# Performance work log

Hardware: AMD Instinct MI355X
Metric: run time of the kernel (lower is better)

## Reference

```python
import jax, jax.numpy as jnp
import numpy as np

M = 12      # max_context_size
H = 768     # hidden_size
NH = 8      # global encoder heads
HD = H // NH
FF = 2048   # global encoder ff_dim
B = 8192


def _gather_hist(buf, mask, idx, ctx):
    """Age-sorted gather of valid circular-buffer slots (oldest first), padded to ctx."""
    Bb, Mx, Hh = buf.shape
    pos = jnp.arange(Mx)
    age = (idx[:, None] - pos[None, :]) % Mx              # [B,M] age of each slot
    key = jnp.where(mask, -age, Mx + 1)                   # valid slots first, oldest (max age) first
    order = jnp.argsort(key, axis=1)                      # stable sort, matches python sorted()
    sorted_buf = jnp.take_along_axis(buf, order[:, :, None], axis=1)
    nvalid = mask.sum(axis=1)                             # [B]
    hist = sorted_buf[:, :ctx]                            # [B,ctx,H]
    valid = jnp.arange(ctx)[None, :] < nvalid[:, None]
    hist = hist * valid[:, :, None]                       # zero out padding rows
    return hist, jnp.minimum(nvalid, ctx)


def _seq_with_current(buf, mask, idx, z_k, ctx):
    """History (ctx-1 slots) + current utterance at the last position (faithful to original,
    including the original's padding-mask behavior arange >= hist_len+1)."""
    Bb = z_k.shape[0]
    hist, hlen = _gather_hist(buf, mask, idx, ctx - 1)
    seq = jnp.concatenate([hist, jnp.zeros((Bb, 1, buf.shape[-1]), buf.dtype)], axis=1)
    seq = seq.at[:, ctx - 1].set(z_k)
    lengths = jnp.minimum(hlen + 1, ctx)
    pad = jnp.arange(ctx)[None, :] >= lengths[:, None]    # True = padded
    return seq, lengths, pad


def _layernorm(x, g, b):
    mu = x.mean(-1, keepdims=True)
    var = x.var(-1, keepdims=True)
    return (x - mu) * jax.lax.rsqrt(var + 1e-5) * g + b


def _forward(z_k, context_buffer, buffer_mask, buffer_indices,
             Wq, bq, Wk, bk, Wv, bv, Wo, bo, ln1_g, ln1_b,
             W1, b1, W2, b2, ln2_g, ln2_b, Wd, bd, Wl, bl, Wg, bg):
    mask = buffer_mask.astype(bool)
    idx = buffer_indices.astype(jnp.int32)
    Bb = z_k.shape[0]

    # ---- global path: 12-slot context -> post-LN transformer layer -> masked mean pool
    gseq, glen, gpad = _seq_with_current(context_buffer, mask, idx, z_k, 12)
    S = 12
    q = (gseq @ Wq + bq).reshape(Bb, S, NH, HD)
    k = (gseq @ Wk + bk).reshape(Bb, S, NH, HD)
    v = (gseq @ Wv + bv).reshape(Bb, S, NH, HD)
    scores = jnp.einsum('bqhd,bkhd->bhqk', q, k) / np.sqrt(HD).astype(np.float32)
    scores = jnp.where(gpad[:, None, None, :], jnp.float32(-1e9), scores)
    attn = jax.nn.softmax(scores, axis=-1)
    ao = jnp.einsum('bhqk,bkhd->bqhd', attn, v).reshape(Bb, S, H) @ Wo + bo
    x = _layernorm(gseq + ao, ln1_g, ln1_b)
    ff = jax.nn.relu(x @ W1 + b1) @ W2 + b2
    x = _layernorm(x + ff, ln2_g, ln2_b)
    gvalid = (~gpad).astype(x.dtype)                       # [B,12]
    denom = jnp.maximum(gvalid.sum(1, keepdims=True), 1.0)
    x_g = (x * gvalid[:, :, None]).sum(1) / denom          # [B,H]

    # ---- direct path
    x_d = jnp.tanh(z_k @ Wd + bd)

    # ---- local path: 5-slot context -> masked mean pool -> projection
    lseq, llen, lpad = _seq_with_current(context_buffer, mask, idx, z_k, 5)
    lvalid = (~lpad).astype(lseq.dtype)
    ldenom = jnp.maximum(lvalid.sum(1, keepdims=True), 1.0)
    lpool = (lseq * lvalid[:, :, None]).sum(1) / ldenom
    x_l = jnp.tanh(lpool @ Wl + bl)

    # ---- gate over [direct, local, global]
    paths = jnp.stack([x_d, x_l, x_g], axis=1)             # [B,3,H]
    logits = paths.reshape(Bb, 3 * H) @ Wg + bg            # [B,3]
    gate = jax.nn.softmax(logits, axis=-1)
    h_k = jnp.einsum('br,brh->bh', gate, paths)
    return h_k


def setup_inputs() -> dict:
    key = jax.random.key(0)
    ks = jax.random.split(key, 24)
    s = 0.02
    inp = {
        'z_k': jax.random.normal(ks[0], (B, H), jnp.float32),
        'context_buffer': jax.random.normal(ks[1], (B, M, H), jnp.float32),
        'buffer_mask': jax.random.randint(ks[2], (B, M), 0, 2, jnp.int32),
        'buffer_indices': jax.random.randint(ks[3], (B,), 0, M, jnp.int32),
        'Wq': jax.random.normal(ks[4], (H, H), jnp.float32) * s,
        'bq': jnp.zeros((H,), jnp.float32),
        'Wk': jax.random.normal(ks[5], (H, H), jnp.float32) * s,
        'bk': jnp.zeros((H,), jnp.float32),
        'Wv': jax.random.normal(ks[6], (H, H), jnp.float32) * s,
        'bv': jnp.zeros((H,), jnp.float32),
        'Wo': jax.random.normal(ks[7], (H, H), jnp.float32) * s,
        'bo': jnp.zeros((H,), jnp.float32),
        'ln1_g': jnp.ones((H,), jnp.float32),
        'ln1_b': jnp.zeros((H,), jnp.float32),
        'W1': jax.random.normal(ks[8], (H, FF), jnp.float32) * s,
        'b1': jnp.zeros((FF,), jnp.float32),
        'W2': jax.random.normal(ks[9], (FF, H), jnp.float32) * s,
        'b2': jnp.zeros((H,), jnp.float32),
        'ln2_g': jnp.ones((H,), jnp.float32),
        'ln2_b': jnp.zeros((H,), jnp.float32),
        'Wd': jax.random.normal(ks[10], (H, H), jnp.float32) * s,
        'bd': jnp.zeros((H,), jnp.float32),
        'Wl': jax.random.normal(ks[11], (H, H), jnp.float32) * s,
        'bl': jnp.zeros((H,), jnp.float32),
        'Wg': jax.random.normal(ks[12], (3 * H, 3), jnp.float32) * s,
        'bg': jnp.zeros((3,), jnp.float32),
    }
    return inp


def reference(z_k, context_buffer, buffer_mask, buffer_indices,
              Wq, bq, Wk, bk, Wv, bv, Wo, bo, ln1_g, ln1_b,
              W1, b1, W2, b2, ln2_g, ln2_b, Wd, bd, Wl, bl, Wg, bg):
    return _forward(z_k, context_buffer, buffer_mask, buffer_indices,
                    Wq, bq, Wk, bk, Wv, bv, Wo, bo, ln1_g, ln1_b,
                    W1, b1, W2, b2, ln2_g, ln2_b, Wd, bd, Wl, bl, Wg, bg)
```

## Files before the change

### kernel.cpp

```cpp
#include <hip/hip_runtime.h>
#include <cstdint>
#include <cstddef>

typedef __bf16 bf16;
typedef __attribute__((ext_vector_type(8))) __bf16 bf16x8;
typedef __attribute__((ext_vector_type(4))) float f32x4;

#define B_TOT 8192

__device__ __forceinline__ void gload16(const void* g, void* l) {
  __builtin_amdgcn_global_load_lds(
      (__attribute__((address_space(1))) void*)g,
      (__attribute__((address_space(3))) void*)l, 16, 0, 0);
}

__device__ __forceinline__ void block_sum2(float& a, float& b, float* lds8) {
#pragma unroll
  for (int o = 32; o; o >>= 1) {
    a += __shfl_xor(a, o, 64);
    b += __shfl_xor(b, o, 64);
  }
  int w = threadIdx.x >> 6;
  if ((threadIdx.x & 63) == 0) { lds8[w] = a; lds8[4 + w] = b; }
  __syncthreads();
  a = lds8[0] + lds8[1] + lds8[2] + lds8[3];
  b = lds8[4] + lds8[5] + lds8[6] + lds8[7];
  __syncthreads();
}

__global__ __launch_bounds__(256) void scan1_kernel(
    const int* __restrict__ mask, int* __restrict__ Lg, int* __restrict__ lbase,
    int* __restrict__ btot, int b0)
{
  __shared__ int ts[256];
  const int t = threadIdx.x;
  const int b = blockIdx.x * 256 + t;
  const int* mp = mask + (long)(b0 + b) * 12;
  int nv = 0;
#pragma unroll
  for (int p = 0; p < 12; ++p) nv += (mp[p] != 0);
  int L = (nv < 11 ? nv : 11) + 1;
  ts[t] = L;
  __syncthreads();
  for (int o = 1; o < 256; o <<= 1) {
    int v = (t >= o) ? ts[t - o] : 0;
    __syncthreads();
    ts[t] += v;
    __syncthreads();
  }
  Lg[b] = L;
  lbase[b] = ts[t] - L;
  if (t == 255) btot[blockIdx.x] = ts[255];
}

__global__ __launch_bounds__(64) void scan2_kernel(
    const int* __restrict__ btot, int* __restrict__ boff, int* __restrict__ meta, int nb)
{
  if (threadIdx.x == 0) {
    int acc = 0;
    for (int i = 0; i < nb; ++i) { int v = btot[i]; boff[i] = acc; acc += v; }
    meta[0] = acc;
  }
}

__global__ __launch_bounds__(256) void prep_kernel(
    const float* __restrict__ z, const float* __restrict__ buf,
    const int* __restrict__ mask, const int* __restrict__ idxs,
    const int* __restrict__ lbase, const int* __restrict__ boff,
    int* __restrict__ fbase, bf16* __restrict__ gseq,
    bf16* __restrict__ zl, int b0, int Bc)
{
  const int bl = blockIdx.x;
  const int b  = b0 + bl;
  __shared__ int ord[12];
  __shared__ int s_nv;
  if (threadIdx.x == 0) {
    int id = idxs[b];
    int nv = 0;
    for (int a = 11; a >= 0; --a) {
      int pos = id - a; if (pos < 0) pos += 12;
      if (mask[b * 12 + pos]) ord[nv++] = pos;
    }
    s_nv = nv;
  }
  const long bs = (long)lbase[bl] + boff[bl >> 8];
  if (threadIdx.x == 0) fbase[bl] = (int)bs;
  __syncthreads();
  const int nv = s_nv;
  const int hg = (nv < 11 ? nv : 11);
  const int hl = (nv < 4 ? nv : 4);
  const float ld = 1.0f / (float)(hl + 1);
  for (int c = threadIdx.x; c < 768; c += 256) {
    float zv = z[(long)b * 768 + c];
    zl[(long)bl * 768 + c] = (bf16)zv;
    float ls = 0.0f;
    for (int s = 0; s < hg; ++s) {
      float v = buf[((long)b * 12 + ord[s]) * 768 + c];
      gseq[(bs + s) * 768 + c] = (bf16)v;
      if (s < hl) ls += v;
    }
    gseq[(bs + hg) * 768 + c] = (hg == 11) ? (bf16)zv : (bf16)0.0f;
    if (nv >= 4) ls += zv;
    zl[((long)Bc + bl) * 768 + c] = (bf16)(ls * ld);
  }
}

__global__ __launch_bounds__(256) void transpose_bf16(
    const float* __restrict__ W, bf16* __restrict__ Wt, int K, int N)
{
  __shared__ float tile[32][33];
  int bn = blockIdx.x * 32;
  int bk = blockIdx.y * 32;
  int tx = threadIdx.x & 31;
  int ty0 = threadIdx.x >> 5;
  for (int ty = ty0; ty < 32; ty += 8)
    tile[ty][tx] = W[(long)(bk + ty) * N + bn + tx];
  __syncthreads();
  for (int ty = ty0; ty < 32; ty += 8)
    Wt[(long)(bn + ty) * K + bk + tx] = (bf16)tile[tx][ty];
}

__global__ __launch_bounds__(256) void pack3_kernel(
    const float* __restrict__ a, const float* __restrict__ b,
    const float* __restrict__ c, float* __restrict__ out)
{
  int t = blockIdx.x * blockDim.x + threadIdx.x;
  if (t < 768) out[t] = a[t];
  else if (t < 1536) out[t] = b[t - 768];
  else if (t < 2304) out[t] = c[t - 1536];
}

__global__ __launch_bounds__(256, 2) void gemm_bt(
    const bf16* __restrict__ A, const bf16* __restrict__ Bt,
    const float* __restrict__ bias, void* __restrict__ C,
    int K, int N, int act, int outf32,
    const int* __restrict__ mlim, int msplit,
    const bf16* __restrict__ Bt2, const float* __restrict__ bias2)
{
  __shared__ __align__(16) bf16 smem[2 * 128 * 64];
  bf16* As = smem;
  bf16* Bs = smem + 128 * 64;
  int gx = gridDim.x, gy = gridDim.y;
  int bx = blockIdx.x, by = blockIdx.y;
  if ((gy & 7) == 0) {
    int l = bx + gx * by;
    int xcd = l & 7, slot = l >> 3;
    bx = slot % gx;
    by = (slot / gx) * 8 + xcd;
  }
  const long m0 = (long)by * 128;
  const long n0 = (long)bx * 128;
  if (mlim && m0 >= mlim[0]) return;
  const bf16* Bsel = (m0 >= msplit) ? Bt2 : Bt;
  const float* bsel = (m0 >= msplit) ? bias2 : bias;

  const int tid  = threadIdx.x;
  const int wave = tid >> 6;
  const int lane = tid & 63;
  const int wm = (wave >> 1) * 64;
  const int wn = (wave & 1) * 64;
  const int i16  = lane & 15;
  const int quad = lane >> 4;
  const int l8 = lane >> 3;
  const int c7 = lane & 7;

  const int csrc = c7 ^ l8;
  const bf16* Ag[4]; const bf16* Bg[4];
  bf16* Al[4]; bf16* Bl[4];
#pragma unroll
  for (int u = 0; u < 4; ++u) {
    int r = wave * 32 + u * 8 + l8;
    Ag[u] = A    + (m0 + r) * K + csrc * 8;
    Bg[u] = Bsel + (n0 + r) * K + csrc * 8;
    Al[u] = As + (wave * 32 + u * 8) * 64 + lane * 8;
    Bl[u] = Bs + (wave * 32 + u * 8) * 64 + lane * 8;
  }

  f32x4 acc[4][4] = {};

  for (int kt = 0; kt < K; kt += 64) {
    __syncthreads();
#pragma unroll
    for (int u = 0; u < 4; ++u) {
      gload16(Ag[u] + kt, Al[u]);
      gload16(Bg[u] + kt, Bl[u]);
    }
    __syncthreads();
#pragma unroll
    for (int s = 0; s < 2; ++s) {
      const int cofs = ((s << 2) | quad) ^ c7;
      bf16x8 af[4], bfr[4];
#pragma unroll
      for (int i = 0; i < 4; ++i)
        af[i] = *(const bf16x8*)(As + (wm + i * 16 + i16) * 64 + cofs * 8);
#pragma unroll
      for (int j = 0; j < 4; ++j)
        bfr[j] = *(const bf16x8*)(Bs + (wn + j * 16 + i16) * 64 + cofs * 8);
#pragma unroll
      for (int i = 0; i < 4; ++i)
#pragma unroll
        for (int j = 0; j < 4; ++j)
          acc[i][j] = __builtin_amdgcn_mfma_f32_16x16x32_bf16(af[i], bfr[j], acc[i][j], 0, 0, 0);
    }
  }

  if (!outf32) {
    __syncthreads();
    bf16* Cs = smem;
#pragma unroll
    for (int j = 0; j < 4; ++j) {
      int col = wn + j * 16 + i16;
      int c8s = (col >> 3) ^ (quad << 1);
      int clo = col & 7;
      float bv = bsel[n0 + col];
#pragma unroll
      for (int i = 0; i < 4; ++i) {
#pragma unroll
        for (int r = 0; r < 4; ++r) {
          int row = wm + i * 16 + quad * 4 + r;
          float v = acc[i][j][r] + bv;
          if (act == 1) v = fmaxf(v, 0.0f);
          Cs[row * 128 + c8s * 8 + clo] = (bf16)v;
        }
      }
    }
    __syncthreads();
    bf16* Cg = (bf16*)C;
#pragma unroll
    for (int u = 0; u < 8; ++u) {
      int g = u * 256 + tid;
      int row = g >> 4, c8 = g & 15;
      int c8s = c8 ^ (((row >> 2) & 3) << 1);
      *(bf16x8*)(Cg + (m0 + row) * N + n0 + c8 * 8) =
          *(const bf16x8*)(Cs + row * 128 + c8s * 8);
    }
  } else {
#pragma unroll
    for (int i = 0; i < 4; ++i) {
#pragma unroll
      for (int j = 0; j < 4; ++j) {
        long col = n0 + wn + j * 16 + i16;
        float bv = bsel[col];
#pragma unroll
        for (int r = 0; r < 4; ++r) {
          long row = m0 + wm + i * 16 + quad * 4 + r;
          float v = acc[i][j][r] + bv;
          if (act == 1) v = fmaxf(v, 0.0f);
          else if (act == 2) v = tanhf(v);
          ((float*)C)[row * N + col] = v;
        }
      }
    }
  }
}

__global__ __launch_bounds__(256, 8) void attn_kernel(
    const bf16* __restrict__ QKV, const int* __restrict__ fbase,
    const int* __restrict__ Lg, bf16* __restrict__ AO)
{
  const int bl  = blockIdx.x;
  const int tid = threadIdx.x;
  const int L   = Lg[bl];
  const long bs = fbase[bl];
  const bf16* qb = QKV + bs * 2304;
  __shared__ bf16 kx[12 * 768];
  __shared__ float att[8][12][12];
  const int LC = L * 96;
  for (int t = tid; t < LC; t += 256) {
    int s = t / 96, c8 = t - s * 96;
    *(bf16x8*)(kx + s * 768 + ((c8 ^ (s & 7)) << 3)) =
        *(const bf16x8*)(qb + (long)s * 2304 + 768 + (c8 << 3));
  }
  __syncthreads();
  const int LL = L * L;
  for (int t = tid; t < 8 * LL; t += 256) {
    int h = t / LL, r = t - h * LL, i = r / L, j = r - (r / L) * L;
    const bf16x8* q = (const bf16x8*)(qb + (long)i * 2304 + h * 96);
    const bf16* kr = kx + j * 768;
    const int cb = h * 12;
    const int jx = j & 7;
    float a = 0.0f;
#pragma unroll
    for (int d = 0; d < 12; ++d) {
      bf16x8 qa = q[d];
      bf16x8 ka = *(const bf16x8*)(kr + (((cb + d) ^ jx) << 3));
#pragma unroll
      for (int e = 0; e < 8; ++e) a += (float)qa[e] * (float)ka[e];
    }
    att[h][i][j] = a * 0.10206207261596575f;
  }
  __syncthreads();
  for (int t = tid; t < 8 * L; t += 256) {
    int h = t / L, i = t - (t / L) * L;
    float mx = -3e38f;
    for (int j = 0; j < L; ++j) mx = fmaxf(mx, att[h][i][j]);
    float sum = 0.0f;
    for (int j = 0; j < L; ++j) { float e = __expf(att[h][i][j] - mx); att[h][i][j] = e; sum += e; }
    float inv = 1.0f / sum;
    for (int j = 0; j < L; ++j) att[h][i][j] *= inv;
  }
  __syncthreads();
  for (int t = tid; t < LC; t += 256) {
    int i = t / 96, c8 = t - i * 96;
    int h = c8 / 12;
    const bf16* vp = qb + 1536 + (c8 << 3);
    float acc[8] = {};
    for (int j = 0; j < L; ++j) {
      float a = att[h][i][j];
      bf16x8 vv = *(const bf16x8*)(vp + (long)j * 2304);
#pragma unroll
      for (int e = 0; e < 8; ++e) acc[e] += a * (float)vv[e];
    }
    bf16x8 o;
#pragma unroll
    for (int e = 0; e < 8; ++e) o[e] = (bf16)acc[e];
    *(bf16x8*)(AO + (bs + i) * 768 + (c8 << 3)) = o;
  }
}

__global__ __launch_bounds__(256) void ln1_kernel(
    const bf16* __restrict__ WoO, const bf16* __restrict__ gseq,
    const float* __restrict__ gam, const float* __restrict__ bet,
    bf16* __restrict__ X, const int* __restrict__ meta)
{
  const long row = blockIdx.x;
  if (row >= meta[0]) return;
  const int tid = threadIdx.x;
  __shared__ float red[8];
  float v[3]; float s = 0.0f, ss = 0.0f;
#pragma unroll
  for (int u = 0; u < 3; ++u) {
    int c = tid + u * 256;
    float x = (float)WoO[row * 768 + c] + (float)gseq[row * 768 + c];
    v[u] = x; s += x; ss += x * x;
  }
  block_sum2(s, ss, red);
  float mu  = s * (1.0f / 768.0f);
  float var = ss * (1.0f / 768.0f) - mu * mu;
  float inv = 1.0f / sqrtf(var + 1e-5f);
#pragma unroll
  for (int u = 0; u < 3; ++u) {
    int c = tid + u * 256;
    X[row * 768 + c] = (bf16)((v[u] - mu) * inv * gam[c] + bet[c]);
  }
}

__global__ __launch_bounds__(256) void ln2gate_kernel(
    const bf16* __restrict__ X, const bf16* __restrict__ FFo,
    const float* __restrict__ gam, const float* __restrict__ bet,
    const int* __restrict__ fbase, const int* __restrict__ Lg,
    const float* __restrict__ xdl, const float* __restrict__ Wg,
    const float* __restrict__ bg, float* __restrict__ out, int b0, int Bc)
{
  const int bl = blockIdx.x;
  const int tid = threadIdx.x;
  const int L = Lg[bl];
  const long bs = fbase[bl];
  __shared__ float red[8];
  __shared__ float red3[12];
  float p0 = 0.0f, p1 = 0.0f, p2 = 0.0f;
  for (int s = 0; s < L; ++s) {
    long row = bs + s;
    float v[3]; float sm = 0.0f, sq = 0.0f;
#pragma unroll
    for (int u = 0; u < 3; ++u) {
      int c = tid + u * 256;
      float x = (float)X[row * 768 + c] + (float)FFo[row * 768 + c];
      v[u] = x; sm += x; sq += x * x;
    }
    block_sum2(sm, sq, red);
    float mu  = sm * (1.0f / 768.0f);
    float var = sq * (1.0f / 768.0f) - mu * mu;
    float inv = 1.0f / sqrtf(var + 1e-5f);
    p0 += (v[0] - mu) * inv * gam[tid]       + bet[tid];
    p1 += (v[1] - mu) * inv * gam[tid + 256] + bet[tid + 256];
    p2 += (v[2] - mu) * inv * gam[tid + 512] + bet[tid + 512];
  }
  float dn = 1.0f / (float)L;
  p0 *= dn; p1 *= dn; p2 *= dn;
  const float* xd = xdl + (long)bl * 768;
  const float* xl = xdl + ((long)Bc + bl) * 768;
  float xd0 = xd[tid], xd1 = xd[tid + 256], xd2 = xd[tid + 512];
  float xl0 = xl[tid], xl1 = xl[tid + 256], xl2 = xl[tid + 512];
  float l0 = 0.0f, l1 = 0.0f, l2 = 0.0f;
#pragma unroll
  for (int r = 0; r < 3; ++r) {
    float lr = xd0 * Wg[tid * 3 + r] + xd1 * Wg[(tid + 256) * 3 + r] + xd2 * Wg[(tid + 512) * 3 + r]
             + xl0 * Wg[(768 + tid) * 3 + r] + xl1 * Wg[(1024 + tid) * 3 + r] + xl2 * Wg[(1280 + tid) * 3 + r]
             + p0 * Wg[(1536 + tid) * 3 + r] + p1 * Wg[(1792 + tid) * 3 + r] + p2 * Wg[(2048 + tid) * 3 + r];
    if (r == 0) l0 = lr; else if (r == 1) l1 = lr; else l2 = lr;
  }
#pragma unroll
  for (int o = 32; o; o >>= 1) {
    l0 += __shfl_xor(l0, o, 64);
    l1 += __shfl_xor(l1, o, 64);
    l2 += __shfl_xor(l2, o, 64);
  }
  if ((tid & 63) == 0) { int w = tid >> 6; red3[w * 3] = l0; red3[w * 3 + 1] = l1; red3[w * 3 + 2] = l2; }
  __syncthreads();
  l0 = red3[0] + red3[3] + red3[6] + red3[9]  + bg[0];
  l1 = red3[1] + red3[4] + red3[7] + red3[10] + bg[1];
  l2 = red3[2] + red3[5] + red3[8] + red3[11] + bg[2];
  float mx = fmaxf(l0, fmaxf(l1, l2));
  float e0 = __expf(l0 - mx), e1 = __expf(l1 - mx), e2 = __expf(l2 - mx);
  float inv = 1.0f / (e0 + e1 + e2);
  e0 *= inv; e1 *= inv; e2 *= inv;
  float* op = out + (long)(b0 + bl) * 768;
  op[tid]       = e0 * xd0 + e1 * xl0 + e2 * p0;
  op[tid + 256] = e0 * xd1 + e1 * xl1 + e2 * p1;
  op[tid + 512] = e0 * xd2 + e1 * xl2 + e2 * p2;
}

extern "C" void kernel_launch(void* const* d_in, const int* in_sizes, int n_in,
                              void* d_out, int out_size, void* d_ws, size_t ws_size,
                              hipStream_t stream) {
  const float* z    = (const float*)d_in[0];
  const float* buf  = (const float*)d_in[1];
  const int*   mask = (const int*)d_in[2];
  const int*   idxs = (const int*)d_in[3];
  const float* Wq = (const float*)d_in[4];  const float* bq = (const float*)d_in[5];
  const float* Wk = (const float*)d_in[6];  const float* bk = (const float*)d_in[7];
  const float* Wv = (const float*)d_in[8];  const float* bv = (const float*)d_in[9];
  const float* Wo = (const float*)d_in[10]; const float* bo = (const float*)d_in[11];
  const float* ln1g = (const float*)d_in[12]; const float* ln1b = (const float*)d_in[13];
  const float* W1 = (const float*)d_in[14]; const float* b1 = (const float*)d_in[15];
  const float* W2 = (const float*)d_in[16]; const float* b2 = (const float*)d_in[17];
  const float* ln2g = (const float*)d_in[18]; const float* ln2b = (const float*)d_in[19];
  const float* Wd = (const float*)d_in[20]; const float* bd = (const float*)d_in[21];
  const float* Wl = (const float*)d_in[22]; const float* blw = (const float*)d_in[23];
  const float* Wg = (const float*)d_in[24]; const float* bg = (const float*)d_in[25];
  float* out = (float*)d_out;
  (void)in_sizes; (void)n_in; (void)out_size;

  auto rnd = [](size_t x) { return (x + 255) & ~(size_t)255; };

  size_t fixed = 0;
  fixed += rnd((size_t)2304 * 768 * 2);
  fixed += rnd((size_t)768 * 768 * 2);
  fixed += rnd((size_t)2048 * 768 * 2);
  fixed += rnd((size_t)768 * 2048 * 2);
  fixed += rnd((size_t)768 * 768 * 2) * 2;
  fixed += rnd((size_t)2304 * 4) + 256 + 512 + 512;

  auto chunkBytes = [&](size_t bc) {
    return rnd((size_t)55296 * bc) + 3 * rnd((size_t)18432 * bc)
         + rnd((size_t)3072 * bc) + rnd((size_t)6144 * bc)
         + 3 * rnd((size_t)4 * bc);
  };
  int Bc = 8192;
  while (Bc > 1024 && fixed + chunkBytes(Bc) > ws_size) Bc >>= 1;

  size_t off = 0;
  auto alloc = [&](size_t n) { void* p = (char*)d_ws + off; off += rnd(n); return p; };
  bf16* Wqkv_t = (bf16*)alloc((size_t)2304 * 768 * 2);
  bf16* Wo_t   = (bf16*)alloc((size_t)768 * 768 * 2);
  bf16* W1_t   = (bf16*)alloc((size_t)2048 * 768 * 2);
  bf16* W2_t   = (bf16*)alloc((size_t)768 * 2048 * 2);
  bf16* Wd_t   = (bf16*)alloc((size_t)768 * 768 * 2);
  bf16* Wl_t   = (bf16*)alloc((size_t)768 * 768 * 2);
  float* bqkv  = (float*)alloc((size_t)2304 * 4);
  int*  meta   = (int*)alloc(256);
  int*  btot   = (int*)alloc(512);
  int*  boff   = (int*)alloc(512);
  bf16* P1 = (bf16*)alloc((size_t)55296 * Bc);
  bf16* P2 = (bf16*)alloc((size_t)18432 * Bc);
  bf16* P3 = (bf16*)alloc((size_t)18432 * Bc);
  bf16* P4 = (bf16*)alloc((size_t)18432 * Bc);
  bf16* zl   = (bf16*)alloc((size_t)3072 * Bc);
  float* xdl = (float*)alloc((size_t)6144 * Bc);
  int*  Lg    = (int*)alloc((size_t)4 * Bc);
  int*  lbase = (int*)alloc((size_t)4 * Bc);
  int*  fbase = (int*)alloc((size_t)4 * Bc);

  transpose_bf16<<<dim3(24, 24), 256, 0, stream>>>(Wq, Wqkv_t,                 768, 768);
  transpose_bf16<<<dim3(24, 24), 256, 0, stream>>>(Wk, Wqkv_t + 768 * 768,     768, 768);
  transpose_bf16<<<dim3(24, 24), 256, 0, stream>>>(Wv, Wqkv_t + 2 * 768 * 768, 768, 768);
  transpose_bf16<<<dim3(24, 24), 256, 0, stream>>>(Wo, Wo_t, 768, 768);
  transpose_bf16<<<dim3(64, 24), 256, 0, stream>>>(W1, W1_t, 768, 2048);
  transpose_bf16<<<dim3(24, 64), 256, 0, stream>>>(W2, W2_t, 2048, 768);
  transpose_bf16<<<dim3(24, 24), 256, 0, stream>>>(Wd, Wd_t, 768, 768);
  transpose_bf16<<<dim3(24, 24), 256, 0, stream>>>(Wl, Wl_t, 768, 768);
  pack3_kernel<<<9, 256, 0, stream>>>(bq, bk, bv, bqkv);

  const int BIG = 0x7fffffff;
  for (int b0 = 0; b0 < B_TOT; b0 += Bc) {
    const int Ycap = (12 * Bc) / 128;
    scan1_kernel<<<Bc / 256, 256, 0, stream>>>(mask, Lg, lbase, btot, b0);
    scan2_kernel<<<1, 64, 0, stream>>>(btot, boff, meta, Bc / 256);
    prep_kernel<<<Bc, 256, 0, stream>>>(z, buf, mask, idxs, lbase, boff, fbase, P2, zl, b0, Bc);
    gemm_bt<<<dim3(6, (2 * Bc) / 128), 256, 0, stream>>>(zl, Wd_t, bd, xdl, 768, 768, 2, 1, nullptr, Bc, Wl_t, blw);
    gemm_bt<<<dim3(18, Ycap), 256, 0, stream>>>(P2, Wqkv_t, bqkv, P1, 768, 2304, 0, 0, meta, BIG, nullptr, nullptr);
    attn_kernel<<<Bc, 256, 0, stream>>>(P1, fbase, Lg, P3);
    gemm_bt<<<dim3(6, Ycap), 256, 0, stream>>>(P3, Wo_t, bo, P4, 768, 768, 0, 0, meta, BIG, nullptr, nullptr);
    ln1_kernel<<<12 * Bc, 256, 0, stream>>>(P4, P2, ln1g, ln1b, P3, meta);
    gemm_bt<<<dim3(16, Ycap), 256, 0, stream>>>(P3, W1_t, b1, P1, 768, 2048, 1, 0, meta, BIG, nullptr, nullptr);
    gemm_bt<<<dim3(6, Ycap), 256, 0, stream>>>(P1, W2_t, b2, P2, 2048, 768, 0, 0, meta, BIG, nullptr, nullptr);
    ln2gate_kernel<<<Bc, 256, 0, stream>>>(P3, P2, ln2g, ln2b, fbase, Lg, xdl, Wg, bg, out, b0, Bc);
  }
}
```

Measured before the change: 1.499 ms.

## Replace 128x128 GEMM with 256x256-tile, 512-thread, multi-stage pipelined GEMM

Swaps the 256-thread 128x128-tile bf16 MFMA GEMM for a 512-thread kernel with 256x256 output tiles. The K loop now steps by 32 through a 4-deep LDS ring buffer, with up to three stages loaded ahead. Next-stage A and B loads are interleaved between the two MFMA halves, and the MFMA sections get raised wave priority. The aim is more operand reuse per byte loaded and better hiding of global-load latency. The cost is 128KB of LDS per block, so at most one block fits per CU. The larger tiles also mean fewer blocks and coarser padding waste on the variable-length M dimension.

```diff
diff --git a/kernel.cpp b/kernel.cpp
--- a/kernel.cpp
+++ b/kernel.cpp
@@ -130,16 +130,15 @@
   else if (t < 2304) out[t] = c[t - 1536];
 }
 
-__global__ __launch_bounds__(256, 2) void gemm_bt(
+__global__ __launch_bounds__(512, 2) void gemm256(
     const bf16* __restrict__ A, const bf16* __restrict__ Bt,
     const float* __restrict__ bias, void* __restrict__ C,
     int K, int N, int act, int outf32,
     const int* __restrict__ mlim, int msplit,
     const bf16* __restrict__ Bt2, const float* __restrict__ bias2)
 {
-  __shared__ __align__(16) bf16 smem[2 * 128 * 64];
-  bf16* As = smem;
-  bf16* Bs = smem + 128 * 64;
+  __shared__ __align__(16) bf16 smem[65536];
+  char* sb = (char*)smem;
   int gx = gridDim.x, gy = gridDim.y;
   int bx = blockIdx.x, by = blockIdx.y;
   if ((gy & 7) == 0) {
@@ -148,103 +147,132 @@
     bx = slot % gx;
     by = (slot / gx) * 8 + xcd;
   }
-  const long m0 = (long)by * 128;
-  const long n0 = (long)bx * 128;
+  const long m0 = (long)by * 256;
+  const long n0 = (long)bx * 256;
   if (mlim && m0 >= mlim[0]) return;
   const bf16* Bsel = (m0 >= msplit) ? Bt2 : Bt;
   const float* bsel = (m0 >= msplit) ? bias2 : bias;
 
   const int tid  = threadIdx.x;
+  const int lane = tid & 63;
   const int wave = tid >> 6;
-  const int lane = tid & 63;
-  const int wm = (wave >> 1) * 64;
-  const int wn = (wave & 1) * 64;
+  const int wm = (wave >> 2) * 128;
+  const int wn = (wave & 3) * 64;
   const int i16  = lane & 15;
   const int quad = lane >> 4;
-  const int l8 = lane >> 3;
-  const int c7 = lane & 7;
-
-  const int csrc = c7 ^ l8;
-  const bf16* Ag[4]; const bf16* Bg[4];
-  bf16* Al[4]; bf16* Bl[4];
-#pragma unroll
-  for (int u = 0; u < 4; ++u) {
-    int r = wave * 32 + u * 8 + l8;
-    Ag[u] = A    + (m0 + r) * K + csrc * 8;
-    Bg[u] = Bsel + (n0 + r) * K + csrc * 8;
-    Al[u] = As + (wave * 32 + u * 8) * 64 + lane * 8;
-    Bl[u] = Bs + (wave * 32 + u * 8) * 64 + lane * 8;
-  }
-
-  f32x4 acc[4][4] = {};
-
-  for (int kt = 0; kt < K; kt += 64) {
-    __syncthreads();
-#pragma unroll
-    for (int u = 0; u < 4; ++u) {
-      gload16(Ag[u] + kt, Al[u]);
-      gload16(Bg[u] + kt, Bl[u]);
-    }
-    __syncthreads();
-#pragma unroll
-    for (int s = 0; s < 2; ++s) {
-      const int cofs = ((s << 2) | quad) ^ c7;
-      bf16x8 af[4], bfr[4];
-#pragma unroll
-      for (int i = 0; i < 4; ++i)
-        af[i] = *(const bf16x8*)(As + (wm + i * 16 + i16) * 64 + cofs * 8);
-#pragma unroll
-      for (int j = 0; j < 4; ++j)
-        bfr[j] = *(const bf16x8*)(Bs + (wn + j * 16 + i16) * 64 + cofs * 8);
-#pragma unroll
-      for (int i = 0; i < 4; ++i)
-#pragma unroll
-        for (int j = 0; j < 4; ++j)
-          acc[i][j] = __builtin_amdgcn_mfma_f32_16x16x32_bf16(af[i], bfr[j], acc[i][j], 0, 0, 0);
-    }
+
+  const int sr = tid >> 2;
+  const int cA = (tid & 3) ^ ((sr >> 1) & 3);
+  const bf16* Ag0 = A    + (m0 + sr) * K + cA * 8;
+  const bf16* Ag1 = A    + (m0 + 128 + sr) * K + cA * 8;
+  const bf16* Bg0 = Bsel + (n0 + sr) * K + cA * 8;
+  const bf16* Bg1 = Bsel + (n0 + 128 + sr) * K + cA * 8;
+  const int ldst = tid << 4;
+
+  const int NK = K >> 5;
+  const int npre = NK < 3 ? NK : 3;
+  for (int s = 0; s < npre; ++s) {
+    char* as_ = sb + ((s & 3) << 14);
+    char* bs_ = sb + 65536 + ((s & 3) << 14);
+    gload16(Ag0 + s * 32, as_ + ldst);
+    gload16(Ag1 + s * 32, as_ + 8192 + ldst);
+    gload16(Bg0 + s * 32, bs_ + ldst);
+    gload16(Bg1 + s * 32, bs_ + 8192 + ldst);
+  }
+
+  const int fc = (quad ^ ((i16 >> 1) & 3)) << 4;
+  f32x4 acc[8][4] = {};
+
+  for (int s = 0; s < NK; ++s) {
+    const char* as_ = sb + ((s & 3) << 14);
+    const char* bs_ = sb + 65536 + ((s & 3) << 14);
+    asm volatile("s_waitcnt vmcnt(8)" ::: "memory");
+    __builtin_amdgcn_s_barrier();
+    bf16x8 a0[4], b0[4];
+#pragma unroll
+    for (int f = 0; f < 4; ++f)
+      a0[f] = *(const bf16x8*)(as_ + (wm + f * 16 + i16) * 64 + fc);
+#pragma unroll
+    for (int g = 0; g < 4; ++g)
+      b0[g] = *(const bf16x8*)(bs_ + (wn + g * 16 + i16) * 64 + fc);
+    if (s + 3 < NK) {
+      char* an = sb + (((s + 3) & 3) << 14);
+      gload16(Ag0 + (s + 3) * 32, an + ldst);
+      gload16(Ag1 + (s + 3) * 32, an + 8192 + ldst);
+    }
+    __builtin_amdgcn_s_barrier();
+    asm volatile("s_waitcnt lgkmcnt(0)" ::: "memory");
+    __builtin_amdgcn_sched_barrier(0);
+    __builtin_amdgcn_s_setprio(1);
+#pragma unroll
+    for (int f = 0; f < 4; ++f)
+#pragma unroll
+      for (int g = 0; g < 4; ++g)
+        acc[f][g] = __builtin_amdgcn_mfma_f32_16x16x32_bf16(a0[f], b0[g], acc[f][g], 0, 0, 0);
+    __builtin_amdgcn_s_setprio(0);
+    __builtin_amdgcn_s_barrier();
+    bf16x8 a1[4];
+#pragma unroll
+    for (int f = 0; f < 4; ++f)
+      a1[f] = *(const bf16x8*)(as_ + (wm + (f + 4) * 16 + i16) * 64 + fc);
+    if (s + 3 < NK) {
+      char* bn = sb + 65536 + (((s + 3) & 3) << 14);
+      gload16(Bg0 + (s + 3) * 32, bn + ldst);
+      gload16(Bg1 + (s + 3) * 32, bn + 8192 + ldst);
+    }
+    __builtin_amdgcn_s_barrier();
+    asm volatile("s_waitcnt lgkmcnt(0)" ::: "memory");
+    __builtin_amdgcn_sched_barrier(0);
+    __builtin_amdgcn_s_setprio(1);
+#pragma unroll
+    for (int f = 0; f < 4; ++f)
+#pragma unroll
+      for (int g = 0; g < 4; ++g)
+        acc[f + 4][g] = __builtin_amdgcn_mfma_f32_16x16x32_bf16(a1[f], b0[g], acc[f + 4][g], 0, 0, 0);
+    __builtin_amdgcn_s_setprio(0);
   }
 
   if (!outf32) {
     __syncthreads();
     bf16* Cs = smem;
 #pragma unroll
-    for (int j = 0; j < 4; ++j) {
-      int col = wn + j * 16 + i16;
+    for (int g = 0; g < 4; ++g) {
+      int col = wn + g * 16 + i16;
       int c8s = (col >> 3) ^ (quad << 1);
       int clo = col & 7;
       float bv = bsel[n0 + col];
 #pragma unroll
-      for (int i = 0; i < 4; ++i) {
+      for (int f = 0; f < 8; ++f) {
 #pragma unroll
         for (int r = 0; r < 4; ++r) {
-          int row = wm + i * 16 + quad * 4 + r;
-          float v = acc[i][j][r] + bv;
+          int row = wm + f * 16 + quad * 4 + r;
+          float v = acc[f][g][r] + bv;
           if (act == 1) v = fmaxf(v, 0.0f);
-          Cs[row * 128 + c8s * 8 + clo] = (bf16)v;
+          Cs[row * 256 + c8s * 8 + clo] = (bf16)v;
         }
       }
     }
     __syncthreads();
     bf16* Cg = (bf16*)C;
 #pragma unroll
-    for (int u = 0; u < 8; ++u) {
-      int g = u * 256 + tid;
-      int row = g >> 4, c8 = g & 15;
+    for (int u = 0; u < 16; ++u) {
+      int g = u * 512 + tid;
+      int row = g >> 5, c8 = g & 31;
       int c8s = c8 ^ (((row >> 2) & 3) << 1);
       *(bf16x8*)(Cg + (m0 + row) * N + n0 + c8 * 8) =
-          *(const bf16x8*)(Cs + row * 128 + c8s * 8);
+          *(const bf16x8*)(Cs + row * 256 + c8s * 8);
     }
   } else {
 #pragma unroll
-    for (int i = 0; i < 4; ++i) {
-#pragma unroll
-      for (int j = 0; j < 4; ++j) {
-        long col = n0 + wn + j * 16 + i16;
+    for (int f = 0; f < 8; ++f) {
+#pragma unroll
+      for (int g = 0; g < 4; ++g) {
+        long col = n0 + wn + g * 16 + i16;
         float bv = bsel[col];
 #pragma unroll
         for (int r = 0; r < 4; ++r) {
-          long row = m0 + wm + i * 16 + quad * 4 + r;
-          float v = acc[i][j][r] + bv;
+          long row = m0 + wm + f * 16 + quad * 4 + r;
+          float v = acc[f][g][r] + bv;
           if (act == 1) v = fmaxf(v, 0.0f);
           else if (act == 2) v = tanhf(v);
           ((float*)C)[row * N + col] = v;
@@ -484,17 +512,17 @@
 
   const int BIG = 0x7fffffff;
   for (int b0 = 0; b0 < B_TOT; b0 += Bc) {
-    const int Ycap = (12 * Bc) / 128;
+    const int Ycap = (12 * Bc) / 256;
     scan1_kernel<<<Bc / 256, 256, 0, stream>>>(mask, Lg, lbase, btot, b0);
     scan2_kernel<<<1, 64, 0, stream>>>(btot, boff, meta, Bc / 256);
     prep_kernel<<<Bc, 256, 0, stream>>>(z, buf, mask, idxs, lbase, boff, fbase, P2, zl, b0, Bc);
-    gemm_bt<<<dim3(6, (2 * Bc) / 128), 256, 0, stream>>>(zl, Wd_t, bd, xdl, 768, 768, 2, 1, nullptr, Bc, Wl_t, blw);
-    gemm_bt<<<dim3(18, Ycap), 256, 0, stream>>>(P2, Wqkv_t, bqkv, P1, 768, 2304, 0, 0, meta, BIG, nullptr, nullptr);
+    gemm256<<<dim3(3, (2 * Bc) / 256), 512, 0, stream>>>(zl, Wd_t, bd, xdl, 768, 768, 2, 1, nullptr, Bc, Wl_t, blw);
+    gemm256<<<dim3(9, Ycap), 512, 0, stream>>>(P2, Wqkv_t, bqkv, P1, 768, 2304, 0, 0, meta, BIG, nullptr, nullptr);
     attn_kernel<<<Bc, 256, 0, stream>>>(P1, fbase, Lg, P3);
-    gemm_bt<<<dim3(6, Ycap), 256, 0, stream>>>(P3, Wo_t, bo, P4, 768, 768, 0, 0, meta, BIG, nullptr, nullptr);
+    gemm256<<<dim3(3, Ycap), 512, 0, stream>>>(P3, Wo_t, bo, P4, 768, 768, 0, 0, meta, BIG, nullptr, nullptr);
     ln1_kernel<<<12 * Bc, 256, 0, stream>>>(P4, P2, ln1g, ln1b, P3, meta);
-    gemm_bt<<<dim3(16, Ycap), 256, 0, stream>>>(P3, W1_t, b1, P1, 768, 2048, 1, 0, meta, BIG, nullptr, nullptr);
-    gemm_bt<<<dim3(6, Ycap), 256, 0, stream>>>(P1, W2_t, b2, P2, 2048, 768, 0, 0, meta, BIG, nullptr, nullptr);
+    gemm256<<<dim3(8, Ycap), 512, 0, stream>>>(P3, W1_t, b1, P1, 768, 2048, 1, 0, meta, BIG, nullptr, nullptr);
+    gemm256<<<dim3(3, Ycap), 512, 0, stream>>>(P1, W2_t, b2, P2, 2048, 768, 0, 0, meta, BIG, nullptr, nullptr);
     ln2gate_kernel<<<Bc, 256, 0, stream>>>(P3, P2, ln2g, ln2b, fbase, Lg, xdl, Wg, bg, out, b0, Bc);
   }
 }
```

Result: slower. 1.534 ms (+2.3%).
